# Kernel tuning notes

Hardware: AMD Instinct MI355X
Metric: run time of the kernel (lower is better)

The kernel has to match this reference:

```python
import jax, jax.numpy as jnp
import numpy as np

EPS = 1e-5
NEG_SLOPE = 0.2

def _bn(h, gamma, beta, axes):
    # training-mode batch norm (batch statistics), matching torch BN forward in train mode
    mu = jnp.mean(h, axis=axes, keepdims=True)
    var = jnp.var(h, axis=axes, keepdims=True)
    return (h - mu) * jax.lax.rsqrt(var + EPS) * gamma + beta

def _lrelu(h):
    return jnp.where(h >= 0, h, NEG_SLOPE * h)

def _edge_conv(x, idx, W, gamma, beta):
    # x: (B,N,C) channels-last; idx: (B,N,k) neighbor indices into N
    # gathered[b,n,j,c] = x[b, idx[b,n,j], c]
    gathered = jnp.take_along_axis(x[:, None, :, :], idx[:, :, :, None], axis=2)  # (B,N,k,C)
    xc = jnp.broadcast_to(x[:, :, None, :], gathered.shape)
    feat = jnp.concatenate([gathered - xc, xc], axis=-1)          # (B,N,k,2C)
    h = jnp.einsum('bnkc,oc->bnko', feat, W)                       # 1x1 conv
    h = _lrelu(_bn(h, gamma, beta, axes=(0, 1, 2)))
    return jnp.max(h, axis=2)                                      # max over k -> (B,N,O)

def setup_inputs() -> dict:
    key = jax.random.key(0)
    ks = jax.random.split(key, 20)
    B, N, K = 8, 2048, 20
    d = {
        'x': jax.random.normal(ks[0], (B, 3, N), jnp.float32),
        'geod_dist': jax.random.normal(ks[1], (B, N, N), jnp.float32),
        'W1': jax.random.normal(ks[2], (64, 6), jnp.float32) * 0.1,
        'g1': jnp.ones((64,)), 'bt1': jnp.zeros((64,)),
        'W2': jax.random.normal(ks[3], (64, 128), jnp.float32) * 0.1,
        'g2': jnp.ones((64,)), 'bt2': jnp.zeros((64,)),
        'W3': jax.random.normal(ks[4], (128, 128), jnp.float32) * 0.1,
        'g3': jnp.ones((128,)), 'bt3': jnp.zeros((128,)),
        'W4': jax.random.normal(ks[5], (256, 256), jnp.float32) * 0.1,
        'g4': jnp.ones((256,)), 'bt4': jnp.zeros((256,)),
        'W5': jax.random.normal(ks[6], (1024, 512), jnp.float32) * 0.05,
        'g5': jnp.ones((1024,)), 'bt5': jnp.zeros((1024,)),
        'L1': jax.random.normal(ks[7], (512, 2048), jnp.float32) * 0.02,
        'g6': jnp.ones((512,)), 'bt6': jnp.zeros((512,)),
        'L2': jax.random.normal(ks[8], (256, 512), jnp.float32) * 0.05,
        'bl2': jnp.zeros((256,)),
        'g7': jnp.ones((256,)), 'bt7': jnp.zeros((256,)),
        'L3': jax.random.normal(ks[9], (40, 256), jnp.float32) * 0.05,
        'bl3': jnp.zeros((40,)),
    }
    return d

def reference(x, geod_dist, W1, g1, bt1, W2, g2, bt2, W3, g3, bt3, W4, g4, bt4,
              W5, g5, bt5, L1, g6, bt6, L2, bl2, g7, bt7, L3, bl3):
    K = 20
    # neighbor indices from geodesic distance (topk largest, as in source)
    idx = jax.lax.top_k(geod_dist, K)[1]            # (B,N,K)
    xt = jnp.transpose(x, (0, 2, 1))                # (B,N,3)
    x1 = _edge_conv(xt, idx, W1, g1, bt1)           # (B,N,64)
    x2 = _edge_conv(x1, idx, W2, g2, bt2)           # (B,N,64)
    x3 = _edge_conv(x2, idx, W3, g3, bt3)           # (B,N,128)
    x4 = _edge_conv(x3, idx, W4, g4, bt4)           # (B,N,256)
    cat = jnp.concatenate([x1, x2, x3, x4], axis=-1)  # (B,N,512)
    h = jnp.einsum('bnc,oc->bno', cat, W5)            # 1x1 conv1d -> (B,N,1024)
    h = _lrelu(_bn(h, g5, bt5, axes=(0, 1)))
    hmax = jnp.max(h, axis=1)                        # (B,1024)
    havg = jnp.mean(h, axis=1)                       # (B,1024)
    z = jnp.concatenate([hmax, havg], axis=1)        # (B,2048)
    z = _lrelu(_bn(z @ L1.T, g6, bt6, axes=(0,)))    # (B,512)
    z = _lrelu(_bn(z @ L2.T + bl2, g7, bt7, axes=(0,)))  # (B,256); dropout = identity (eval)
    return z @ L3.T + bl3                            # (B,40)
```

## Files before the change

### kernel.cpp

```cpp
#include <hip/hip_runtime.h>
#include <hip/hip_bf16.h>
#include <cstdint>
#include <cstddef>

#define NB 8
#define NP 2048
#define NK 20
#define BN 16384

typedef _Float16 half8 __attribute__((ext_vector_type(8)));
typedef _Float16 half4v __attribute__((ext_vector_type(4)));
typedef float f32x4 __attribute__((ext_vector_type(4)));

__device__ __forceinline__ void gload_lds16(const void* g, void* l) {
  __builtin_amdgcn_global_load_lds(
      (const __attribute__((address_space(1))) unsigned int*)g,
      (__attribute__((address_space(3))) unsigned int*)l, 16, 0, 0);
}

static constexpr size_t OFF_IDX   = 0;
static constexpr size_t OFF_XT    = OFF_IDX + (size_t)BN*NK*4;
static constexpr size_t OFF_XCATH = OFF_XT + (size_t)BN*3*4;
static constexpr size_t OFF_WT1   = OFF_XCATH + (size_t)BN*512*2;
static constexpr size_t OFF_WD1   = OFF_WT1 + 3*64*4;
static constexpr size_t OFF_BC2   = OFF_WD1 + 3*64*4;
static constexpr size_t OFF_BC3   = OFF_BC2 + (size_t)64*128*2;
static constexpr size_t OFF_BC4   = OFF_BC3 + (size_t)64*256*2;
static constexpr size_t OFF_B5    = OFF_BC4 + (size_t)128*512*2;
static constexpr size_t OFF_YH    = OFF_B5 + (size_t)512*1024*2;
static constexpr size_t OFF_HSEL  = OFF_YH + (size_t)BN*512*2;
static constexpr size_t OFF_SPARE = OFF_HSEL + (size_t)BN*256*4;
static constexpr size_t OFF_H5    = OFF_HSEL;
static constexpr size_t OFF_PART  = OFF_SPARE + (size_t)BN*256*4;
static constexpr size_t OFF_PMEAN = OFF_PART + (size_t)8*1024*1024;
static constexpr size_t OFF_SS    = OFF_PMEAN + (size_t)8*8*1024*4;
static constexpr size_t OFF_Z     = OFF_SS + 2*1024*4;
static constexpr size_t OFF_Z1P   = OFF_Z + (size_t)NB*2048*4;
static constexpr size_t OFF_Z2P   = OFF_Z1P + NB*512*4;

__device__ __forceinline__ void prep_b_dev(const float* __restrict__ W,
                                           _Float16* __restrict__ Bp, int t,
                                           int K2, int lgO, int lgRS) {
  int O = 1 << lgO;
  int o = t & (O - 1), k = t >> lgO;
  float v = W[((size_t)o << lgRS) + k];
  int ch = k >> 6, ks = (k >> 5) & 1, kg = (k >> 3) & 3, e = k & 7;
  int sl = o >> 4, ol = o & 15;
  size_t flat = (((size_t)(ch * 2 + ks) * (O >> 4) + sl) * 64 + (kg * 16 + ol)) * 8 + e;
  Bp[flat] = (_Float16)v;
}

__device__ __forceinline__ void prep_bc_dev(const float* __restrict__ W,
                                            _Float16* __restrict__ Bp, int t,
                                            int C, int lgO2, int lgRS) {
  int O2 = 1 << lgO2, O = O2 >> 1;
  int o2 = t & (O2 - 1), k = t >> lgO2;
  float v;
  if (o2 < O) v = W[((size_t)o2 << lgRS) + k];
  else {
    int o = o2 - O;
    v = W[((size_t)o << lgRS) + C + k] - W[((size_t)o << lgRS) + k];
  }
  int ch = k >> 6, ks = (k >> 5) & 1, kg = (k >> 3) & 3, e = k & 7;
  int sl = o2 >> 4, ol = o2 & 15;
  size_t flat = (((size_t)(ch * 2 + ks) * (O2 >> 4) + sl) * 64 + (kg * 16 + ol)) * 8 + e;
  Bp[flat] = (_Float16)v;
}

__device__ __forceinline__ unsigned fmap(float x) {
  unsigned b = __float_as_uint(x);
  return b ^ (unsigned)(((int)b >> 31) | 0x80000000);
}

#define INS3U(u, gi, m1, i1, m2, i2, m3, i3)             \
  {                                                      \
    bool c1 = (u) > m1;                                  \
    unsigned t_ = c1 ? m1 : (u); int ti_ = c1 ? i1 : (gi);\
    m1 = c1 ? (u) : m1;          i1 = c1 ? (gi) : i1;    \
    bool c2 = t_ > m2;                                   \
    unsigned t2_ = c2 ? m2 : t_; int t2i_ = c2 ? i2 : ti_;\
    m2 = c2 ? t_ : m2;           i2 = c2 ? ti_ : i2;     \
    bool c3 = t2_ > m3;                                  \
    m3 = c3 ? t2_ : m3;          i3 = c3 ? t2i_ : i3;    \
  }

#define SCAN3U(uv, m1, i1, m2, i2, m3, i3)                             \
  _Pragma("unroll")                                                    \
  for (int r = 0; r < 8; ++r) {                                        \
    _Pragma("unroll")                                                  \
    for (int e = 0; e < 4; ++e) {                                      \
      unsigned val = uv[r][e];                                         \
      int gi = r * 256 + l * 4 + e;                                    \
      INS3U(val, gi, m1, i1, m2, i2, m3, i3)                           \
    }                                                                  \
  }

#define SCAN3UM(uv, dead, m1, i1, m2, i2, m3, i3)                      \
  _Pragma("unroll")                                                    \
  for (int r = 0; r < 8; ++r) {                                        \
    _Pragma("unroll")                                                  \
    for (int e = 0; e < 4; ++e) {                                      \
      int el = r * 4 + e;                                              \
      unsigned val = ((dead >> el) & 1u) ? 0u : uv[r][e];              \
      int gi = r * 256 + l * 4 + e;                                    \
      INS3U(val, gi, m1, i1, m2, i2, m3, i3)                           \
    }                                                                  \
  }

template <int CTRL>
__device__ __forceinline__ void dpp_pair_max(unsigned& hi, unsigned& lo) {
  unsigned h2 = (unsigned)__builtin_amdgcn_update_dpp((int)hi, (int)hi, CTRL, 0xF, 0xF, false);
  unsigned l2 = (unsigned)__builtin_amdgcn_update_dpp((int)lo, (int)lo, CTRL, 0xF, 0xF, false);
  bool take = (h2 > hi) || (h2 == hi && l2 > lo);
  hi = take ? h2 : hi;
  lo = take ? l2 : lo;
}

__device__ __forceinline__ void topk_row(const float* __restrict__ g,
                                         int* __restrict__ out, int l) {
  unsigned uv[8][4];
#pragma unroll
  for (int r = 0; r < 8; ++r) {
    float4 v = *(const float4*)&g[r * 256 + l * 4];
    uv[r][0] = fmap(v.x); uv[r][1] = fmap(v.y);
    uv[r][2] = fmap(v.z); uv[r][3] = fmap(v.w);
  }
  unsigned int dead = 0;
  unsigned m1 = 0, m2 = 0, m3 = 0;
  int i1 = 0, i2 = 0, i3 = 0;
  SCAN3U(uv, m1, i1, m2, i2, m3, i3)
  for (int it = 0; it < NK; ++it) {
    unsigned hi = m1, lo = ~(unsigned)i1;
    dpp_pair_max<0x111>(hi, lo);
    dpp_pair_max<0x112>(hi, lo);
    dpp_pair_max<0x114>(hi, lo);
    dpp_pair_max<0x118>(hi, lo);
    dpp_pair_max<0x142>(hi, lo);
    dpp_pair_max<0x143>(hi, lo);
    int best_i = ~(unsigned)__builtin_amdgcn_readlane((int)lo, 63);
    if (l == 0) out[it] = best_i;
    if (((best_i >> 2) & 63) == l) {
      dead |= 1u << (((best_i >> 8) << 2) | (best_i & 3));
      m1 = m2; i1 = i2; m2 = m3; i2 = i3; m3 = 0; i3 = 0;
      if (m1 == 0) { SCAN3UM(uv, dead, m1, i1, m2, i2, m3, i3) }
    }
  }
}

static constexpr int PB_TR  = 0;
static constexpr int PB_W1  = PB_TR + 192;
static constexpr int PB_BC2 = PB_W1 + 1;
static constexpr int PB_BC3 = PB_BC2 + 32;
static constexpr int PB_BC4 = PB_BC3 + 64;
static constexpr int PB_B5  = PB_BC4 + 256;
static constexpr int PB_END = PB_B5 + 2048;
static constexpr int PB_TOPK_END = PB_END + BN / 4;

__global__ __launch_bounds__(256) void k_prep_topk(
    const float* __restrict__ x, float* __restrict__ xt,
    const float* __restrict__ W1, float* __restrict__ wt1, float* __restrict__ wd1,
    const float* __restrict__ W2, _Float16* __restrict__ bc2,
    const float* __restrict__ W3, _Float16* __restrict__ bc3,
    const float* __restrict__ W4, _Float16* __restrict__ bc4,
    const float* __restrict__ W5, _Float16* __restrict__ b5,
    const float* __restrict__ geod, int* __restrict__ idx) {
  int blk = blockIdx.x, tid = threadIdx.x;
  if (blk >= PB_END) {
    int wv = tid >> 6, l = tid & 63;
    int row = (blk - PB_END) * 4 + wv;
    topk_row(geod + (size_t)row * NP, idx + (size_t)row * NK, l);
    return;
  }
  if (blk < PB_W1) {
    int t = blk * 256 + tid;
    int n = t & (NP - 1);
    int c = (t / NP) % 3;
    int b = t / (3 * NP);
    xt[(size_t)(b * NP + n) * 3 + c] = x[t];
  } else if (blk < PB_BC2) {
    int t = tid;
    if (t < 192) {
      int o = t & 63, c = t >> 6;
      float w0 = W1[o * 6 + c];
      float w1 = W1[o * 6 + 3 + c];
      wt1[c * 64 + o] = w0;
      wd1[c * 64 + o] = w1 - w0;
    }
  } else if (blk < PB_BC3) prep_bc_dev(W2, bc2, (blk - PB_BC2) * 256 + tid, 64, 7, 7);
  else if (blk < PB_BC4)   prep_bc_dev(W3, bc3, (blk - PB_BC3) * 256 + tid, 64, 8, 7);
  else if (blk < PB_B5)    prep_bc_dev(W4, bc4, (blk - PB_BC4) * 256 + tid, 128, 9, 8);
  else                     prep_b_dev(W5, b5,   (blk - PB_B5) * 256 + tid, 512, 10, 9);
}

__global__ __launch_bounds__(256) void k_edge1(
    const float* __restrict__ xt, const int* __restrict__ idx,
    const float* __restrict__ wt1, const float* __restrict__ wd1,
    const float* __restrict__ gamma,
    float* __restrict__ hsel, float* __restrict__ part) {
  __shared__ float xl[NP * 3];
  __shared__ int lidx[32 * NK];
  __shared__ float red[256];
  int tid = threadIdx.x;
  int b = blockIdx.x >> 6;
  int grp = blockIdx.x & 63;
  int p0 = grp * 32;
  for (int u = tid; u < NP * 3; u += 256) xl[u] = xt[(size_t)b * NP * 3 + u];
  for (int u = tid; u < 32 * NK; u += 256) lidx[u] = idx[((size_t)b * NP + p0) * NK + u];
  __syncthreads();
  int o = tid & 63;
  int pb = tid >> 6;
  float w0 = wt1[o], w1 = wt1[64 + o], w2 = wt1[128 + o];
  float d0 = wd1[o], d1 = wd1[64 + o], d2 = wd1[128 + o];
  bool pos = gamma[o] >= 0.f;
  float ps = 0.f, ps2 = 0.f;
#pragma unroll
  for (int i = 0; i < 8; ++i) {
    int pp = pb * 8 + i;
    int p = p0 + pp;
    float base = xl[p * 3] * d0 + xl[p * 3 + 1] * d1 + xl[p * 3 + 2] * d2;
    float mx = -3.4e38f, mn = 3.4e38f;
    for (int j = 0; j < NK; ++j) {
      int nb = lidx[pp * NK + j];
      float h = base + xl[nb * 3] * w0 + xl[nb * 3 + 1] * w1 + xl[nb * 3 + 2] * w2;
      mx = fmaxf(mx, h); mn = fminf(mn, h);
      ps += h; ps2 += h * h;
    }
    size_t P = (size_t)b * NP + p;
    hsel[P * 64 + o] = pos ? mx : mn;
  }
  red[tid] = ps;
  __syncthreads();
  if (tid < 64) {
    float a = red[tid] + red[64 + tid] + red[128 + tid] + red[192 + tid];
    part[(size_t)blockIdx.x * 64 + tid] = a;
  }
  __syncthreads();
  red[tid] = ps2;
  __syncthreads();
  if (tid < 64) {
    float a = red[tid] + red[64 + tid] + red[128 + tid] + red[192 + tid];
    part[((size_t)gridDim.x + blockIdx.x) * 64 + tid] = a;
  }
}

template <int C, int O2, int NSPLIT>
__global__ __launch_bounds__(256) void k_dense_mfma(
    const _Float16* __restrict__ xh, int in_off,
    const _Float16* __restrict__ Bp, _Float16* __restrict__ yH) {
  constexpr int NCH = C / 64;
  constexpr int NO = O2 / NSPLIT;
  constexpr int NSLO = NO / 16;
  constexpr int NS = NSLO / 2;
  constexpr int PAIRS = 2 * NSLO;
  __shared__ __align__(16) _Float16 ldsA[64 * 64];
  __shared__ __align__(16) _Float16 ldsB[PAIRS * 512];
  int tid = threadIdx.x, wv = tid >> 6, l = tid & 63;
  int mblk = blockIdx.x, nid = 0;
  if (NSPLIT > 1) { nid = mblk >> 8; mblk &= 255; }
  int m0 = mblk * 64;
  int n_base = nid * NO;
  int mg = wv & 1, ng = wv >> 1;
  f32x4 acc[2][NS];
#pragma unroll
  for (int m = 0; m < 2; ++m)
#pragma unroll
    for (int s = 0; s < NS; ++s)
#pragma unroll
      for (int r = 0; r < 4; ++r) acc[m][s][r] = 0.f;

  for (int ch = 0; ch < NCH; ++ch) {
#pragma unroll
    for (int it = 0; it < 2; ++it) {
      int r0 = wv * 16 + it * 8;
      int R = r0 + (l >> 3);
      int q = (l & 7) ^ (l >> 3);
      gload_lds16(xh + (size_t)(m0 + R) * 512 + in_off + ch * 64 + q * 8, ldsA + r0 * 64);
    }
    for (int u = wv; u < PAIRS; u += 4) {
      int ks = u / NSLO, sloc = u - ks * NSLO;
      gload_lds16(Bp + ((size_t)((ch * 2 + ks) * (O2 / 16) + (n_base >> 4) + sloc) * 64 + l) * 8,
                  ldsB + u * 512);
    }
    __syncthreads();
#pragma unroll
    for (int ks = 0; ks < 2; ++ks) {
      half8 b[NS];
#pragma unroll
      for (int s = 0; s < NS; ++s)
        b[s] = *(const half8*)(ldsB + (ks * NSLO + ng * NS + s) * 512 + l * 8);
#pragma unroll
      for (int mt = 0; mt < 2; ++mt) {
        int row = mg * 32 + mt * 16 + (l & 15);
        int slot = (ks * 4 + (l >> 4)) ^ (row & 7);
        half8 a = *(const half8*)(ldsA + row * 64 + slot * 8);
#pragma unroll
        for (int s = 0; s < NS; ++s)
          acc[mt][s] = __builtin_amdgcn_mfma_f32_16x16x32_f16(a, b[s], acc[mt][s], 0, 0, 0);
      }
    }
    __syncthreads();
  }
  int g = l >> 4;
#pragma unroll
  for (int s = 0; s < NS; ++s) {
    int col = n_base + ng * (NS * 16) + s * 16 + (l & 15);
#pragma unroll
    for (int mt = 0; mt < 2; ++mt)
#pragma unroll
      for (int r = 0; r < 4; ++r) {
        int row = m0 + mg * 32 + mt * 16 + 4 * g + r;
        yH[(size_t)row * O2 + col] = (_Float16)acc[mt][s][r];
      }
  }
}

template <int O>
__global__ __launch_bounds__(256) void k_gather(
    const _Float16* __restrict__ yH, const int* __restrict__ idx,
    const float* __restrict__ gamma,
    float* __restrict__ hsel, float* __restrict__ part) {
  constexpr int O2 = 2 * O;
  constexpr int CG = O / 4;
  constexpr int PPB = 256 / CG;
  __shared__ int lidx[PPB * NK];
  __shared__ float4 redS[256], redQ[256];
  int tid = threadIdx.x;
  int p0 = blockIdx.x * PPB;
  int bbase = p0 & ~(NP - 1);
  for (int u = tid; u < PPB * NK; u += 256) lidx[u] = idx[(size_t)p0 * NK + u];
  __syncthreads();
  int pp = tid / CG, g = tid - pp * CG;
  int p = p0 + pp;
  half4v sb4 = *(const half4v*)&yH[(size_t)p * O2 + O + g * 4];
  float sb[4] = {(float)sb4[0], (float)sb4[1], (float)sb4[2], (float)sb4[3]};
  float4 gv = *(const float4*)&gamma[g * 4];
  float mx[4], mn[4], sm[4], sq[4];
#pragma unroll
  for (int e = 0; e < 4; ++e) { mx[e] = -3.4e38f; mn[e] = 3.4e38f; sm[e] = 0.f; sq[e] = 0.f; }
#pragma unroll
  for (int j = 0; j < NK; ++j) {
    int nb = bbase + lidx[pp * NK + j];
    half4v y4 = *(const half4v*)&yH[(size_t)nb * O2 + g * 4];
#pragma unroll
    for (int e = 0; e < 4; ++e) {
      float h = (float)y4[e] + sb[e];
      mx[e] = fmaxf(mx[e], h); mn[e] = fminf(mn[e], h);
      sm[e] += h; sq[e] += h * h;
    }
  }
  float s0 = (gv.x >= 0.f) ? mx[0] : mn[0];
  float s1 = (gv.y >= 0.f) ? mx[1] : mn[1];
  float s2 = (gv.z >= 0.f) ? mx[2] : mn[2];
  float s3 = (gv.w >= 0.f) ? mx[3] : mn[3];
  *(float4*)&hsel[(size_t)p * O + g * 4] = make_float4(s0, s1, s2, s3);
  redS[tid] = make_float4(sm[0], sm[1], sm[2], sm[3]);
  redQ[tid] = make_float4(sq[0], sq[1], sq[2], sq[3]);
  __syncthreads();
  if (tid < CG) {
    float4 a = redS[tid], q = redQ[tid];
    for (int k = 1; k < PPB; ++k) {
      float4 b = redS[tid + k * CG], c = redQ[tid + k * CG];
      a.x += b.x; a.y += b.y; a.z += b.z; a.w += b.w;
      q.x += c.x; q.y += c.y; q.z += c.z; q.w += c.w;
    }
    *(float4*)&part[(size_t)blockIdx.x * O + tid * 4] = a;
    *(float4*)&part[((size_t)gridDim.x + blockIdx.x) * O + tid * 4] = q;
  }
}

__global__ __launch_bounds__(256) void k_conv5_mfma(
    const _Float16* __restrict__ xh, const _Float16* __restrict__ Bp,
    const float* __restrict__ gamma,
    _Float16* __restrict__ h5, float* __restrict__ part) {
  __shared__ __align__(16) _Float16 ldsA[64 * 64];
  __shared__ __align__(16) _Float16 ldsB[32 * 512];
  __shared__ float ldsS[2][256], ldsQ[2][256], ldsMx[2][256], ldsMn[2][256];
  int tid = threadIdx.x, wv = tid >> 6, l = tid & 63;
  int mblk = blockIdx.x & 255, nid = blockIdx.x >> 8;
  int m0 = mblk * 64;
  int n_base = nid * 256;
  int mg = wv & 1, ng = wv >> 1;
  f32x4 acc[2][8];
#pragma unroll
  for (int m = 0; m < 2; ++m)
#pragma unroll
    for (int s = 0; s < 8; ++s)
#pragma unroll
      for (int r = 0; r < 4; ++r) acc[m][s][r] = 0.f;

  for (int ch = 0; ch < 8; ++ch) {
#pragma unroll
    for (int it = 0; it < 2; ++it) {
      int r0 = wv * 16 + it * 8;
      int R = r0 + (l >> 3);
      int q = (l & 7) ^ (l >> 3);
      gload_lds16(xh + (size_t)(m0 + R) * 512 + ch * 64 + q * 8, ldsA + r0 * 64);
    }
    for (int u = wv; u < 32; u += 4) {
      int ks = u >> 4, sloc = u & 15;
      gload_lds16(Bp + ((size_t)((ch * 2 + ks) * 64 + (n_base >> 4) + sloc) * 64 + l) * 8,
                  ldsB + u * 512);
    }
    __syncthreads();
#pragma unroll
    for (int ks = 0; ks < 2; ++ks) {
      half8 b[8];
#pragma unroll
      for (int s = 0; s < 8; ++s)
        b[s] = *(const half8*)(ldsB + (ks * 16 + ng * 8 + s) * 512 + l * 8);
#pragma unroll
      for (int mt = 0; mt < 2; ++mt) {
        int row = mg * 32 + mt * 16 + (l & 15);
        int slot = (ks * 4 + (l >> 4)) ^ (row & 7);
        half8 a = *(const half8*)(ldsA + row * 64 + slot * 8);
#pragma unroll
        for (int s = 0; s < 8; ++s)
          acc[mt][s] = __builtin_amdgcn_mfma_f32_16x16x32_f16(a, b[s], acc[mt][s], 0, 0, 0);
      }
    }
    __syncthreads();
  }
  int g = l >> 4;
#pragma unroll
  for (int s = 0; s < 8; ++s) {
    float sm = 0.f, sq = 0.f, mx = -3.4e38f, mn = 3.4e38f;
    int col = n_base + ng * 128 + s * 16 + (l & 15);
#pragma unroll
    for (int mt = 0; mt < 2; ++mt)
#pragma unroll
      for (int r = 0; r < 4; ++r) {
        float v = acc[mt][s][r];
        int row = m0 + mg * 32 + mt * 16 + 4 * g + r;
        h5[(size_t)row * 1024 + col] = (_Float16)v;
        sm += v; sq += v * v; mx = fmaxf(mx, v); mn = fminf(mn, v);
      }
    sm += __shfl_xor(sm, 16); sm += __shfl_xor(sm, 32);
    sq += __shfl_xor(sq, 16); sq += __shfl_xor(sq, 32);
    mx = fmaxf(mx, __shfl_xor(mx, 16)); mx = fmaxf(mx, __shfl_xor(mx, 32));
    mn = fminf(mn, __shfl_xor(mn, 16)); mn = fminf(mn, __shfl_xor(mn, 32));
    if (l < 16) {
      int u = ng * 128 + s * 16 + l;
      ldsS[mg][u] = sm; ldsQ[mg][u] = sq; ldsMx[mg][u] = mx; ldsMn[mg][u] = mn;
    }
  }
  __syncthreads();
  {
    int u = tid;
    int col = n_base + u;
    part[(size_t)mblk * 1024 + col] = ldsS[0][u] + ldsS[1][u];
    part[((size_t)256 + mblk) * 1024 + col] = ldsQ[0][u] + ldsQ[1][u];
    float sel = (gamma[col] >= 0.f) ? fmaxf(ldsMx[0][u], ldsMx[1][u])
                                    : fminf(ldsMn[0][u], ldsMn[1][u]);
    part[((size_t)512 + mblk) * 1024 + col] = sel;
  }
}

__global__ __launch_bounds__(256) void k_finalize(
    const float* __restrict__ part, int G, int O, float inv_count,
    const float* __restrict__ gamma, const float* __restrict__ beta,
    float* __restrict__ ss) {
  int o = blockIdx.x;
  float s = 0.f, s2 = 0.f;
  for (int g = threadIdx.x; g < G; g += 256) {
    s  += part[(size_t)g * O + o];
    s2 += part[((size_t)G + g) * O + o];
  }
#pragma unroll
  for (int sft = 32; sft; sft >>= 1) {
    s  += __shfl_down(s, sft);
    s2 += __shfl_down(s2, sft);
  }
  __shared__ float aw[4], aw2[4];
  int w = threadIdx.x >> 6;
  if ((threadIdx.x & 63) == 0) { aw[w] = s; aw2[w] = s2; }
  __syncthreads();
  if (threadIdx.x == 0) {
    s = aw[0] + aw[1] + aw[2] + aw[3];
    s2 = aw2[0] + aw2[1] + aw2[2] + aw2[3];
    float m   = s * inv_count;
    float var = s2 * inv_count - m * m;
    float scale = gamma[o] * rsqrtf(var + 1e-5f);
    ss[o]     = scale;
    ss[O + o] = beta[o] - m * scale;
  }
}

__global__ void k_edge_apply(const float* __restrict__ hsel,
                             const float* __restrict__ ss, _Float16* __restrict__ xh,
                             int O, int off) {
  int t = blockIdx.x * 256 + threadIdx.x;
  int cgn = O >> 2;
  int gq = t % cgn;
  int p = t / cgn;
  int o = gq * 4;
  float4 sc = *(const float4*)&ss[o];
  float4 sh = *(const float4*)&ss[O + o];
  float4 v = *(const float4*)&hsel[(size_t)p * O + o];
  float y0 = sc.x * v.x + sh.x; y0 = (y0 >= 0.f) ? y0 : 0.2f * y0;
  float y1 = sc.y * v.y + sh.y; y1 = (y1 >= 0.f) ? y1 : 0.2f * y1;
  float y2 = sc.z * v.z + sh.z; y2 = (y2 >= 0.f) ? y2 : 0.2f * y2;
  float y3 = sc.w * v.w + sh.w; y3 = (y3 >= 0.f) ? y3 : 0.2f * y3;
  half4v out;
  out[0] = (_Float16)y0; out[1] = (_Float16)y1;
  out[2] = (_Float16)y2; out[3] = (_Float16)y3;
  *(half4v*)&xh[(size_t)p * 512 + off + o] = out;
}

__global__ __launch_bounds__(256) void k_pool5a(const _Float16* __restrict__ h5,
                                                const float* __restrict__ ss,
                                                float* __restrict__ pmean) {
  int bi = blockIdx.x;
  int b = bi >> 5, ns = (bi >> 2) & 7, cg = bi & 3;
  int col = cg * 256 + threadIdx.x;
  float scale = ss[col], shift = ss[1024 + col];
  float sm = 0.f;
  for (int n = ns * 256; n < ns * 256 + 256; ++n) {
    float v = (float)h5[(size_t)(b * 2048 + n) * 1024 + col];
    float y = scale * v + shift;
    y = (y >= 0.f) ? y : 0.2f * y;
    sm += y;
  }
  pmean[(size_t)(b * 8 + ns) * 1024 + col] = sm;
}

__global__ __launch_bounds__(256) void k_pool5b(const float* __restrict__ part,
                                                const float* __restrict__ pmean,
                                                const float* __restrict__ ss,
                                                float* __restrict__ z) {
  int bi = blockIdx.x;
  int b = bi >> 2, cg = bi & 3;
  int col = cg * 256 + threadIdx.x;
  float scale = ss[col], shift = ss[1024 + col];
  const float* psel = part + (size_t)512 * 1024;
  bool pos = scale >= 0.f;
  float hv = pos ? -3.4e38f : 3.4e38f;
  for (int q = 0; q < 32; ++q) {
    float v = psel[(size_t)(b * 32 + q) * 1024 + col];
    hv = pos ? fmaxf(hv, v) : fminf(hv, v);
  }
  float zmax = scale * hv + shift;
  zmax = (zmax >= 0.f) ? zmax : 0.2f * zmax;
  float sm = 0.f;
  for (int ns = 0; ns < 8; ++ns) sm += pmean[(size_t)(b * 8 + ns) * 1024 + col];
  z[b * 2048 + col] = zmax;
  z[b * 2048 + 1024 + col] = sm * (1.f / 2048.f);
}

__global__ __launch_bounds__(64) void k_fc(const float* __restrict__ in,
                                           const float* __restrict__ Wf,
                                           float* __restrict__ out, int IN, int O) {
  int blk = blockIdx.x;
  int b = blk / O, o = blk % O;
  const float4* a = (const float4*)(in + (size_t)b * IN);
  const float4* w = (const float4*)(Wf + (size_t)o * IN);
  float s = 0.f;
  for (int i = threadIdx.x; i < (IN >> 2); i += 64) {
    float4 av = a[i], wv = w[i];
    s += av.x * wv.x + av.y * wv.y + av.z * wv.z + av.w * wv.w;
  }
#pragma unroll
  for (int sft = 32; sft; sft >>= 1) s += __shfl_down(s, sft);
  if (threadIdx.x == 0) out[(size_t)b * O + o] = s;
}

__global__ __launch_bounds__(256) void k_fc2bn(
    const float* __restrict__ z1p,
    const float* __restrict__ g6, const float* __restrict__ bt6,
    const float* __restrict__ L2, const float* __restrict__ bl2,
    float* __restrict__ z2p) {
  __shared__ float z1[NB * 512];
  int tid = threadIdx.x;
  for (int u = tid; u < NB * 512; u += 256) z1[u] = z1p[u];
  __syncthreads();
#pragma unroll
  for (int cc = 0; cc < 2; ++cc) {
    int c = tid + cc * 256;
    float s = 0.f, s2 = 0.f;
#pragma unroll
    for (int b = 0; b < NB; ++b) {
      float v = z1[b * 512 + c];
      s += v; s2 += v * v;
    }
    float m = s * (1.f / NB);
    float var = s2 * (1.f / NB) - m * m;
    float scale = g6[c] * rsqrtf(var + 1e-5f);
    float shift = bt6[c] - m * scale;
#pragma unroll
    for (int b = 0; b < NB; ++b) {
      float y = scale * z1[b * 512 + c] + shift;
      z1[b * 512 + c] = (y >= 0.f) ? y : 0.2f * y;
    }
  }
  __syncthreads();
  int wv = tid >> 6, l = tid & 63;
  int u = blockIdx.x * 4 + wv;
  int b = u >> 8, o = u & 255;
  const float4* a = (const float4*)&z1[b * 512];
  const float4* w = (const float4*)(L2 + (size_t)o * 512);
  float s = 0.f;
#pragma unroll
  for (int i = l; i < 128; i += 64) {
    float4 av = a[i], wvv = w[i];
    s += av.x * wvv.x + av.y * wvv.y + av.z * wvv.z + av.w * wvv.w;
  }
#pragma unroll
  for (int sft = 32; sft; sft >>= 1) s += __shfl_down(s, sft);
  if (l == 0) z2p[u] = s + bl2[o];
}

__global__ __launch_bounds__(256) void k_fc3bn(
    const float* __restrict__ z2p,
    const float* __restrict__ g7, const float* __restrict__ bt7,
    const float* __restrict__ L3, const float* __restrict__ bl3,
    float* __restrict__ out) {
  __shared__ float z2[NB * 256];
  int tid = threadIdx.x;
  for (int u = tid; u < NB * 256; u += 256) z2[u] = z2p[u];
  __syncthreads();
  {
    int c = tid;
    float s = 0.f, s2 = 0.f;
#pragma unroll
    for (int b = 0; b < NB; ++b) {
      float v = z2[b * 256 + c];
      s += v; s2 += v * v;
    }
    float m = s * (1.f / NB);
    float var = s2 * (1.f / NB) - m * m;
    float scale = g7[c] * rsqrtf(var + 1e-5f);
    float shift = bt7[c] - m * scale;
#pragma unroll
    for (int b = 0; b < NB; ++b) {
      float y = scale * z2[b * 256 + c] + shift;
      z2[b * 256 + c] = (y >= 0.f) ? y : 0.2f * y;
    }
  }
  __syncthreads();
  int wv = tid >> 6, l = tid & 63;
  int u = blockIdx.x * 4 + wv;
  int b = u / 40, o = u - b * 40;
  const float4* a = (const float4*)&z2[b * 256];
  const float4* w = (const float4*)(L3 + (size_t)o * 256);
  float s = 0.f;
  {
    float4 av = a[l], wvv = w[l];
    s += av.x * wvv.x + av.y * wvv.y + av.z * wvv.z + av.w * wvv.w;
  }
#pragma unroll
  for (int sft = 32; sft; sft >>= 1) s += __shfl_down(s, sft);
  if (l == 0) out[u] = s + bl3[o];
}

extern "C" void kernel_launch(void* const* d_in, const int* in_sizes, int n_in,
                              void* d_out, int out_size, void* d_ws, size_t ws_size,
                              hipStream_t stream) {
  (void)in_sizes; (void)n_in; (void)out_size; (void)ws_size;
  const float* x    = (const float*)d_in[0];
  const float* geod = (const float*)d_in[1];
  const float* W1   = (const float*)d_in[2];
  const float* g1   = (const float*)d_in[3];
  const float* bt1  = (const float*)d_in[4];
  const float* W2   = (const float*)d_in[5];
  const float* g2   = (const float*)d_in[6];
  const float* bt2  = (const float*)d_in[7];
  const float* W3   = (const float*)d_in[8];
  const float* g3   = (const float*)d_in[9];
  const float* bt3  = (const float*)d_in[10];
  const float* W4   = (const float*)d_in[11];
  const float* g4   = (const float*)d_in[12];
  const float* bt4  = (const float*)d_in[13];
  const float* W5   = (const float*)d_in[14];
  const float* g5   = (const float*)d_in[15];
  const float* bt5  = (const float*)d_in[16];
  const float* L1   = (const float*)d_in[17];
  const float* g6   = (const float*)d_in[18];
  const float* bt6  = (const float*)d_in[19];
  const float* L2   = (const float*)d_in[20];
  const float* bl2  = (const float*)d_in[21];
  const float* g7   = (const float*)d_in[22];
  const float* bt7  = (const float*)d_in[23];
  const float* L3   = (const float*)d_in[24];
  const float* bl3  = (const float*)d_in[25];

  char* ws = (char*)d_ws;
  int*       idx   = (int*)(ws + OFF_IDX);
  float*     xt    = (float*)(ws + OFF_XT);
  _Float16*  xcatH = (_Float16*)(ws + OFF_XCATH);
  float*     wt1   = (float*)(ws + OFF_WT1);
  float*     wd1   = (float*)(ws + OFF_WD1);
  _Float16*  bc2   = (_Float16*)(ws + OFF_BC2);
  _Float16*  bc3   = (_Float16*)(ws + OFF_BC3);
  _Float16*  bc4   = (_Float16*)(ws + OFF_BC4);
  _Float16*  b5    = (_Float16*)(ws + OFF_B5);
  _Float16*  yH    = (_Float16*)(ws + OFF_YH);
  float*     hsel  = (float*)(ws + OFF_HSEL);
  _Float16*  h5    = (_Float16*)(ws + OFF_H5);
  float*     part  = (float*)(ws + OFF_PART);
  float*     pmean = (float*)(ws + OFF_PMEAN);
  float*     ssb   = (float*)(ws + OFF_SS);
  float*     z     = (float*)(ws + OFF_Z);
  float*     z1p   = (float*)(ws + OFF_Z1P);
  float*     z2p   = (float*)(ws + OFF_Z2P);

  const float invE = 1.f / (float)(BN * NK);
  const float inv5 = 1.f / (float)(BN);

  k_prep_topk<<<PB_TOPK_END, 256, 0, stream>>>(x, xt, W1, wt1, wd1,
                                               W2, bc2, W3, bc3, W4, bc4, W5, b5,
                                               geod, idx);

  k_edge1<<<512, 256, 0, stream>>>(xt, idx, wt1, wd1, g1, hsel, part);
  k_finalize<<<64, 256, 0, stream>>>(part, 512, 64, invE, g1, bt1, ssb);
  k_edge_apply<<<(BN * 64) / 1024, 256, 0, stream>>>(hsel, ssb, xcatH, 64, 0);
  k_dense_mfma<64, 128, 1><<<256, 256, 0, stream>>>(xcatH, 0, bc2, yH);
  k_gather<64><<<BN / 16, 256, 0, stream>>>(yH, idx, g2, hsel, part);
  k_finalize<<<64, 256, 0, stream>>>(part, BN / 16, 64, invE, g2, bt2, ssb);
  k_edge_apply<<<(BN * 64) / 1024, 256, 0, stream>>>(hsel, ssb, xcatH, 64, 64);
  k_dense_mfma<64, 256, 1><<<256, 256, 0, stream>>>(xcatH, 64, bc3, yH);
  k_gather<128><<<BN / 8, 256, 0, stream>>>(yH, idx, g3, hsel, part);
  k_finalize<<<128, 256, 0, stream>>>(part, BN / 8, 128, invE, g3, bt3, ssb);
  k_edge_apply<<<(BN * 128) / 1024, 256, 0, stream>>>(hsel, ssb, xcatH, 128, 128);
  k_dense_mfma<128, 512, 2><<<512, 256, 0, stream>>>(xcatH, 128, bc4, yH);
  k_gather<256><<<BN / 4, 256, 0, stream>>>(yH, idx, g4, hsel, part);
  k_finalize<<<256, 256, 0, stream>>>(part, BN / 4, 256, invE, g4, bt4, ssb);
  k_edge_apply<<<(BN * 256) / 1024, 256, 0, stream>>>(hsel, ssb, xcatH, 256, 256);

  k_conv5_mfma<<<1024, 256, 0, stream>>>(xcatH, b5, g5, h5, part);
  k_finalize<<<1024, 256, 0, stream>>>(part, 256, 1024, inv5, g5, bt5, ssb);
  k_pool5a<<<256, 256, 0, stream>>>(h5, ssb, pmean);
  k_pool5b<<<32, 256, 0, stream>>>(part, pmean, ssb, z);

  k_fc<<<NB * 512, 64, 0, stream>>>(z, L1, z1p, 2048, 512);
  k_fc2bn<<<NB * 256 / 4, 256, 0, stream>>>(z1p, g6, bt6, L2, bl2, z2p);
  k_fc3bn<<<NB * 40 / 4, 256, 0, stream>>>(z2p, g7, bt7, L3, bl3, (float*)d_out);
}
```

Measured before the change: 233.6 us.

## Enlarge conv5 M tile, reorder topk blocks first, fp16 L1 weights

The conv5 MFMA kernel now handles 128 rows per block instead of 64, which halves the grid and doubles the accumulator registers. The aim is to reuse the B tile across more rows. The prep/topk kernel now schedules its topk blocks ahead of the prep blocks and also converts L1 to fp16. The FC1 kernel then reads half the weight bytes. The risks are higher register pressure and lower occupancy in conv5, plus reduced precision in FC1.

```diff
diff --git a/kernel.cpp b/kernel.cpp
--- a/kernel.cpp
+++ b/kernel.cpp
@@ -37,6 +37,7 @@
 static constexpr size_t OFF_Z     = OFF_SS + 2*1024*4;
 static constexpr size_t OFF_Z1P   = OFF_Z + (size_t)NB*2048*4;
 static constexpr size_t OFF_Z2P   = OFF_Z1P + NB*512*4;
+static constexpr size_t OFF_L1H   = OFF_Z2P + (size_t)NB*256*4;
 
 __device__ __forceinline__ void prep_b_dev(const float* __restrict__ W,
                                            _Float16* __restrict__ Bp, int t,
@@ -147,14 +148,15 @@
   }
 }
 
+static constexpr int NTOPK = BN / 4;
 static constexpr int PB_TR  = 0;
 static constexpr int PB_W1  = PB_TR + 192;
 static constexpr int PB_BC2 = PB_W1 + 1;
 static constexpr int PB_BC3 = PB_BC2 + 32;
 static constexpr int PB_BC4 = PB_BC3 + 64;
 static constexpr int PB_B5  = PB_BC4 + 256;
-static constexpr int PB_END = PB_B5 + 2048;
-static constexpr int PB_TOPK_END = PB_END + BN / 4;
+static constexpr int PB_L1H = PB_B5 + 2048;
+static constexpr int PB_END = PB_L1H + 4096;
 
 __global__ __launch_bounds__(256) void k_prep_topk(
     const float* __restrict__ x, float* __restrict__ xt,
@@ -163,14 +165,16 @@
     const float* __restrict__ W3, _Float16* __restrict__ bc3,
     const float* __restrict__ W4, _Float16* __restrict__ bc4,
     const float* __restrict__ W5, _Float16* __restrict__ b5,
+    const float* __restrict__ L1, _Float16* __restrict__ l1h,
     const float* __restrict__ geod, int* __restrict__ idx) {
   int blk = blockIdx.x, tid = threadIdx.x;
-  if (blk >= PB_END) {
+  if (blk < NTOPK) {
     int wv = tid >> 6, l = tid & 63;
-    int row = (blk - PB_END) * 4 + wv;
+    int row = blk * 4 + wv;
     topk_row(geod + (size_t)row * NP, idx + (size_t)row * NK, l);
     return;
   }
+  blk -= NTOPK;
   if (blk < PB_W1) {
     int t = blk * 256 + tid;
     int n = t & (NP - 1);
@@ -189,7 +193,11 @@
   } else if (blk < PB_BC3) prep_bc_dev(W2, bc2, (blk - PB_BC2) * 256 + tid, 64, 7, 7);
   else if (blk < PB_BC4)   prep_bc_dev(W3, bc3, (blk - PB_BC3) * 256 + tid, 64, 8, 7);
   else if (blk < PB_B5)    prep_bc_dev(W4, bc4, (blk - PB_BC4) * 256 + tid, 128, 9, 8);
-  else                     prep_b_dev(W5, b5,   (blk - PB_B5) * 256 + tid, 512, 10, 9);
+  else if (blk < PB_L1H)   prep_b_dev(W5, b5,   (blk - PB_B5) * 256 + tid, 512, 10, 9);
+  else {
+    int t = (blk - PB_L1H) * 256 + tid;
+    l1h[t] = (_Float16)L1[t];
+  }
 }
 
 __global__ __launch_bounds__(256) void k_edge1(
@@ -372,17 +380,17 @@
     const _Float16* __restrict__ xh, const _Float16* __restrict__ Bp,
     const float* __restrict__ gamma,
     _Float16* __restrict__ h5, float* __restrict__ part) {
-  __shared__ __align__(16) _Float16 ldsA[64 * 64];
+  __shared__ __align__(16) _Float16 ldsA[128 * 64];
   __shared__ __align__(16) _Float16 ldsB[32 * 512];
   __shared__ float ldsS[2][256], ldsQ[2][256], ldsMx[2][256], ldsMn[2][256];
   int tid = threadIdx.x, wv = tid >> 6, l = tid & 63;
-  int mblk = blockIdx.x & 255, nid = blockIdx.x >> 8;
-  int m0 = mblk * 64;
+  int mblk = blockIdx.x & 127, nid = blockIdx.x >> 7;
+  int m0 = mblk * 128;
   int n_base = nid * 256;
   int mg = wv & 1, ng = wv >> 1;
-  f32x4 acc[2][8];
-#pragma unroll
-  for (int m = 0; m < 2; ++m)
+  f32x4 acc[4][8];
+#pragma unroll
+  for (int m = 0; m < 4; ++m)
 #pragma unroll
     for (int s = 0; s < 8; ++s)
 #pragma unroll
@@ -390,8 +398,8 @@
 
   for (int ch = 0; ch < 8; ++ch) {
 #pragma unroll
-    for (int it = 0; it < 2; ++it) {
-      int r0 = wv * 16 + it * 8;
+    for (int it = 0; it < 4; ++it) {
+      int r0 = wv * 32 + it * 8;
       int R = r0 + (l >> 3);
       int q = (l & 7) ^ (l >> 3);
       gload_lds16(xh + (size_t)(m0 + R) * 512 + ch * 64 + q * 8, ldsA + r0 * 64);
@@ -409,8 +417,8 @@
       for (int s = 0; s < 8; ++s)
         b[s] = *(const half8*)(ldsB + (ks * 16 + ng * 8 + s) * 512 + l * 8);
 #pragma unroll
-      for (int mt = 0; mt < 2; ++mt) {
-        int row = mg * 32 + mt * 16 + (l & 15);
+      for (int mt = 0; mt < 4; ++mt) {
+        int row = mg * 64 + mt * 16 + (l & 15);
         int slot = (ks * 4 + (l >> 4)) ^ (row & 7);
         half8 a = *(const half8*)(ldsA + row * 64 + slot * 8);
 #pragma unroll
@@ -426,11 +434,11 @@
     float sm = 0.f, sq = 0.f, mx = -3.4e38f, mn = 3.4e38f;
     int col = n_base + ng * 128 + s * 16 + (l & 15);
 #pragma unroll
-    for (int mt = 0; mt < 2; ++mt)
+    for (int mt = 0; mt < 4; ++mt)
 #pragma unroll
       for (int r = 0; r < 4; ++r) {
         float v = acc[mt][s][r];
-        int row = m0 + mg * 32 + mt * 16 + 4 * g + r;
+        int row = m0 + mg * 64 + mt * 16 + 4 * g + r;
         h5[(size_t)row * 1024 + col] = (_Float16)v;
         sm += v; sq += v * v; mx = fmaxf(mx, v); mn = fminf(mn, v);
       }
@@ -448,10 +456,10 @@
     int u = tid;
     int col = n_base + u;
     part[(size_t)mblk * 1024 + col] = ldsS[0][u] + ldsS[1][u];
-    part[((size_t)256 + mblk) * 1024 + col] = ldsQ[0][u] + ldsQ[1][u];
+    part[((size_t)128 + mblk) * 1024 + col] = ldsQ[0][u] + ldsQ[1][u];
     float sel = (gamma[col] >= 0.f) ? fmaxf(ldsMx[0][u], ldsMx[1][u])
                                     : fminf(ldsMn[0][u], ldsMn[1][u]);
-    part[((size_t)512 + mblk) * 1024 + col] = sel;
+    part[((size_t)256 + mblk) * 1024 + col] = sel;
   }
 }
 
@@ -531,11 +539,11 @@
   int b = bi >> 2, cg = bi & 3;
   int col = cg * 256 + threadIdx.x;
   float scale = ss[col], shift = ss[1024 + col];
-  const float* psel = part + (size_t)512 * 1024;
+  const float* psel = part + (size_t)256 * 1024;
   bool pos = scale >= 0.f;
   float hv = pos ? -3.4e38f : 3.4e38f;
-  for (int q = 0; q < 32; ++q) {
-    float v = psel[(size_t)(b * 32 + q) * 1024 + col];
+  for (int q = 0; q < 16; ++q) {
+    float v = psel[(size_t)(b * 16 + q) * 1024 + col];
     hv = pos ? fmaxf(hv, v) : fminf(hv, v);
   }
   float zmax = scale * hv + shift;
@@ -547,16 +555,18 @@
 }
 
 __global__ __launch_bounds__(64) void k_fc(const float* __restrict__ in,
-                                           const float* __restrict__ Wf,
+                                           const _Float16* __restrict__ Wf,
                                            float* __restrict__ out, int IN, int O) {
   int blk = blockIdx.x;
   int b = blk / O, o = blk % O;
   const float4* a = (const float4*)(in + (size_t)b * IN);
-  const float4* w = (const float4*)(Wf + (size_t)o * IN);
+  const half8* w = (const half8*)(Wf + (size_t)o * IN);
   float s = 0.f;
-  for (int i = threadIdx.x; i < (IN >> 2); i += 64) {
-    float4 av = a[i], wv = w[i];
-    s += av.x * wv.x + av.y * wv.y + av.z * wv.z + av.w * wv.w;
+  for (int i = threadIdx.x; i < (IN >> 3); i += 64) {
+    half8 wv = w[i];
+    float4 a0 = a[2 * i], a1 = a[2 * i + 1];
+    s += a0.x * (float)wv[0] + a0.y * (float)wv[1] + a0.z * (float)wv[2] + a0.w * (float)wv[3]
+       + a1.x * (float)wv[4] + a1.y * (float)wv[5] + a1.z * (float)wv[6] + a1.w * (float)wv[7];
   }
 #pragma unroll
   for (int sft = 32; sft; sft >>= 1) s += __shfl_down(s, sft);
@@ -701,13 +711,14 @@
   float*     z     = (float*)(ws + OFF_Z);
   float*     z1p   = (float*)(ws + OFF_Z1P);
   float*     z2p   = (float*)(ws + OFF_Z2P);
+  _Float16*  l1h   = (_Float16*)(ws + OFF_L1H);
 
   const float invE = 1.f / (float)(BN * NK);
   const float inv5 = 1.f / (float)(BN);
 
-  k_prep_topk<<<PB_TOPK_END, 256, 0, stream>>>(x, xt, W1, wt1, wd1,
-                                               W2, bc2, W3, bc3, W4, bc4, W5, b5,
-                                               geod, idx);
+  k_prep_topk<<<NTOPK + PB_END, 256, 0, stream>>>(x, xt, W1, wt1, wd1,
+                                                  W2, bc2, W3, bc3, W4, bc4, W5, b5,
+                                                  L1, l1h, geod, idx);
 
   k_edge1<<<512, 256, 0, stream>>>(xt, idx, wt1, wd1, g1, hsel, part);
   k_finalize<<<64, 256, 0, stream>>>(part, 512, 64, invE, g1, bt1, ssb);
@@ -725,12 +736,12 @@
   k_finalize<<<256, 256, 0, stream>>>(part, BN / 4, 256, invE, g4, bt4, ssb);
   k_edge_apply<<<(BN * 256) / 1024, 256, 0, stream>>>(hsel, ssb, xcatH, 256, 256);
 
-  k_conv5_mfma<<<1024, 256, 0, stream>>>(xcatH, b5, g5, h5, part);
-  k_finalize<<<1024, 256, 0, stream>>>(part, 256, 1024, inv5, g5, bt5, ssb);
+  k_conv5_mfma<<<512, 256, 0, stream>>>(xcatH, b5, g5, h5, part);
+  k_finalize<<<1024, 256, 0, stream>>>(part, 128, 1024, inv5, g5, bt5, ssb);
   k_pool5a<<<256, 256, 0, stream>>>(h5, ssb, pmean);
   k_pool5b<<<32, 256, 0, stream>>>(part, pmean, ssb, z);
 
-  k_fc<<<NB * 512, 64, 0, stream>>>(z, L1, z1p, 2048, 512);
+  k_fc<<<NB * 512, 64, 0, stream>>>(z, l1h, z1p, 2048, 512);
   k_fc2bn<<<NB * 256 / 4, 256, 0, stream>>>(z1p, g6, bt6, L2, bl2, z2p);
   k_fc3bn<<<NB * 40 / 4, 256, 0, stream>>>(z2p, g7, bt7, L3, bl3, (float*)d_out);
 }
```

Result: no change. 236.6 us (+1.3%).
